# Performance work log

Measured on AMD Instinct MI355X. Metric: run time of the kernel, lower is better.

## Reference

```python
import jax, jax.numpy as jnp
import numpy as np

B, S, E, H = 1, 2048, 2048, 32
D = E // H  # head_dim = 64
QMAX = 127.0


def _ste(x, xq):
    # straight-through fake quant (forward = xq, grad = identity)
    return x + jax.lax.stop_gradient(xq - x)


def fake_quant_act(x):
    # per-tensor symmetric int8 fake quantization (QuantMatMul.quant_x*/act quantizer)
    scale = jnp.maximum(jnp.max(jnp.abs(x)) / QMAX, 1e-8)
    xq = jnp.clip(jnp.round(x / scale), -128.0, QMAX) * scale
    return _ste(x, xq)


def fake_quant_weight(w):
    # per-output-channel symmetric int8 fake quantization (weight quantizer)
    scale = jnp.maximum(jnp.max(jnp.abs(w), axis=1, keepdims=True) / QMAX, 1e-8)
    wq = jnp.clip(jnp.round(w / scale), -128.0, QMAX) * scale
    return _ste(w, wq)


def rope_cos_sin(seq_len, dim):
    inv_freq = 1.0 / (10000.0 ** (jnp.arange(0, dim, 2, dtype=jnp.float32) / dim))
    t = jnp.arange(seq_len, dtype=jnp.float32)
    freqs = jnp.outer(t, inv_freq)            # [S, D/2]
    emb = jnp.concatenate([freqs, freqs], -1)  # [S, D]
    return jnp.cos(emb), jnp.sin(emb)


def rotate_half(x):
    x1, x2 = jnp.split(x, 2, axis=-1)
    return jnp.concatenate([-x2, x1], axis=-1)


def setup_inputs() -> dict:
    key = jax.random.key(0)
    ks = jax.random.split(key, 5)
    return {
        "hidden_states": jax.random.normal(ks[0], (B, S, E), dtype=jnp.float32),
        "w_q": jax.random.normal(ks[1], (E, E), dtype=jnp.float32) * 0.02,
        "w_k": jax.random.normal(ks[2], (E, E), dtype=jnp.float32) * 0.02,
        "w_v": jax.random.normal(ks[3], (E, E), dtype=jnp.float32) * 0.02,
        "w_o": jax.random.normal(ks[4], (E, E), dtype=jnp.float32) * 0.02,
    }


def reference(hidden_states, w_q, w_k, w_v, w_o):
    scaling = D ** -0.5
    # quantized projections (QuantLinear: fake-quant weight, no input quant for q/k/v)
    q = hidden_states @ fake_quant_weight(w_q).T * scaling
    k = hidden_states @ fake_quant_weight(w_k).T
    v = hidden_states @ fake_quant_weight(w_v).T
    # qkt_matmul.quant_x1/quant_x2, pv_matmul.quant_x2
    q = fake_quant_act(q)
    k = fake_quant_act(k)
    v = fake_quant_act(v)
    # [B,S,E] -> [B,H,S,D]
    q = q.reshape(B, S, H, D).transpose(0, 2, 1, 3)
    k = k.reshape(B, S, H, D).transpose(0, 2, 1, 3)
    v = v.reshape(B, S, H, D).transpose(0, 2, 1, 3)
    # rotary embedding
    cos, sin = rope_cos_sin(S, D)
    cos = cos[None, None]
    sin = sin[None, None]
    q = q * cos + rotate_half(q) * sin
    k = k * cos + rotate_half(k) * sin
    # QK^T (already scaled via q) + causal mask
    scores = jnp.einsum("bhsd,bhtd->bhst", q, k)  # [B,H,S,S]
    causal = jnp.tril(jnp.ones((S, S), dtype=bool))
    scores = jnp.where(causal[None, None], scores, jnp.finfo(scores.dtype).min)
    probs = jax.nn.softmax(scores.astype(jnp.float32), axis=-1).astype(q.dtype)
    # PV matmul (v already fake-quantized)
    out = jnp.einsum("bhst,bhtd->bhsd", probs, v)
    out = out.transpose(0, 2, 1, 3).reshape(B, S, E)
    # o_proj: QuantLinear with input quant enabled
    out = fake_quant_act(out) @ fake_quant_weight(w_o).T
    return out
```

## Files before the change

### kernel.cpp

```cpp
#include <hip/hip_runtime.h>
#include <hip/hip_bf16.h>
#include <hip/hip_fp16.h>

#define S_LEN 2048
#define E_DIM 2048
#define H_NUM 32
#define D_DIM 64

typedef __attribute__((ext_vector_type(8))) short short8;
typedef __attribute__((ext_vector_type(4))) short short4v;
typedef __attribute__((ext_vector_type(4))) float f32x4;
typedef __attribute__((ext_vector_type(4))) int i32x4;

__device__ __forceinline__ unsigned short f2h(float f) {
  return __builtin_bit_cast(unsigned short, (_Float16)f);
}

__device__ __forceinline__ float h2f(unsigned short u) {
  return (float)__builtin_bit_cast(_Float16, u);
}

__device__ __forceinline__ float fq1(float x, float invs, float scale) {
  return fminf(fmaxf(rintf(x * invs), -128.f), 127.f) * scale;
}

__device__ __forceinline__ int q8(float x, float invs) {
  return min(max((int)rintf(x * invs), -128), 127);
}

__device__ __forceinline__ void gload_lds16(const void* g, void* l) {
  __builtin_amdgcn_global_load_lds((const __attribute__((address_space(1))) void*)g,
                                   (__attribute__((address_space(3))) void*)l, 16, 0, 0);
}

__device__ __forceinline__ f32x4 mfma16h(short8 a, short8 b, f32x4 c) {
  return __builtin_amdgcn_mfma_f32_16x16x32_f16(a, b, c, 0, 0, 0);
}

__device__ __forceinline__ i32x4 mfma16i8(i32x4 a, i32x4 b, i32x4 c) {
  return __builtin_amdgcn_mfma_i32_16x16x64_i8(a, b, c, 0, 0, 0);
}

#define VMW4() asm volatile("s_waitcnt vmcnt(4)" ::: "memory")
#define VMW3() asm volatile("s_waitcnt vmcnt(3)" ::: "memory")
#define VMW2() asm volatile("s_waitcnt vmcnt(2)" ::: "memory")
#define VMW0() asm volatile("s_waitcnt vmcnt(0)" ::: "memory")
#define BARR() asm volatile("s_barrier" ::: "memory")

__global__ void k_prep(const float* __restrict__ hs,
                       const float* __restrict__ w_q, const float* __restrict__ w_k,
                       const float* __restrict__ w_v, const float* __restrict__ w_o,
                       unsigned short* __restrict__ hsb, unsigned short* __restrict__ wq_all,
                       signed char* __restrict__ wo_i8, float* __restrict__ wsc,
                       unsigned* __restrict__ sc, float2* __restrict__ trig) {
  const int b = blockIdx.x;
  if (b < 4096) {
    int i = b * 256 + threadIdx.x;
    float4 v = ((const float4*)hs)[i];
    ushort4 r;
    r.x = f2h(v.x); r.y = f2h(v.y); r.z = f2h(v.z); r.w = f2h(v.w);
    ((ushort4*)hsb)[i] = r;
    return;
  }
  if (b >= 12288) {
    if (b == 12288) {
      if (threadIdx.x < 8) sc[threadIdx.x] = 0u;
      return;
    }
    int idx = (b - 12289) * 256 + threadIdx.x;
    int s = idx >> 5, i = idx & 31;
    float freq = exp2f(-(float)i * (13.287712379549449f / 32.f));
    float ang = (float)s * freq;
    float sn, cs;
    sincosf(ang, &sn, &cs);
    float2 t; t.x = cs; t.y = sn;
    trig[idx] = t;
    return;
  }
  __shared__ float wm[4];
  const int isWo = (b >= 10240);
  const int bb = isWo ? (b - 10240) : (b - 4096);
  const int wy = isWo ? 0 : (bb >> 11);
  const int wx = isWo ? bb : (bb & 2047);
  const float* w = isWo ? w_o : (wy == 0 ? w_q : wy == 1 ? w_k : w_v);
  const float* row = w + (size_t)wx * E_DIM;
  float4 a = ((const float4*)row)[threadIdx.x * 2];
  float4 bq = ((const float4*)row)[threadIdx.x * 2 + 1];
  float m = fmaxf(fmaxf(fmaxf(fabsf(a.x), fabsf(a.y)), fmaxf(fabsf(a.z), fabsf(a.w))),
                  fmaxf(fmaxf(fabsf(bq.x), fabsf(bq.y)), fmaxf(fabsf(bq.z), fabsf(bq.w))));
#pragma unroll
  for (int off = 32; off; off >>= 1) m = fmaxf(m, __shfl_xor(m, off));
  if ((threadIdx.x & 63) == 0) wm[threadIdx.x >> 6] = m;
  __syncthreads();
  m = fmaxf(fmaxf(wm[0], wm[1]), fmaxf(wm[2], wm[3]));
  float scale = fmaxf(m * (1.f / 127.f), 1e-8f);
  float invs = 1.f / scale;
  if (isWo) {
    unsigned lo = (unsigned)(q8(a.x, invs) & 255) | ((unsigned)(q8(a.y, invs) & 255) << 8) |
                  ((unsigned)(q8(a.z, invs) & 255) << 16) | ((unsigned)(q8(a.w, invs) & 255) << 24);
    unsigned hi = (unsigned)(q8(bq.x, invs) & 255) | ((unsigned)(q8(bq.y, invs) & 255) << 8) |
                  ((unsigned)(q8(bq.z, invs) & 255) << 16) | ((unsigned)(q8(bq.w, invs) & 255) << 24);
    uint2 pk; pk.x = lo; pk.y = hi;
    ((uint2*)(wo_i8 + (size_t)wx * E_DIM))[threadIdx.x] = pk;
    if (threadIdx.x == 0) wsc[wx] = scale;
  } else {
    unsigned short* orow = wq_all + (size_t)wy * E_DIM * E_DIM + (size_t)wx * E_DIM;
    ushort4 r0, r1;
    r0.x = f2h(fq1(a.x, invs, scale)); r0.y = f2h(fq1(a.y, invs, scale));
    r0.z = f2h(fq1(a.z, invs, scale)); r0.w = f2h(fq1(a.w, invs, scale));
    r1.x = f2h(fq1(bq.x, invs, scale)); r1.y = f2h(fq1(bq.y, invs, scale));
    r1.z = f2h(fq1(bq.z, invs, scale)); r1.w = f2h(fq1(bq.w, invs, scale));
    ((ushort4*)orow)[threadIdx.x * 2] = r0;
    ((ushort4*)orow)[threadIdx.x * 2 + 1] = r1;
  }
}

__global__ __launch_bounds__(256, 3)
void k_gemm_qkv(const unsigned short* __restrict__ A, const unsigned short* __restrict__ Bt,
                unsigned short* __restrict__ C, unsigned* __restrict__ amax, float alpha_q) {
  __shared__ char lds[49152];
  const int K = 2048, NT = 64;
  const int lin = blockIdx.z * 256 + blockIdx.y * 16 + blockIdx.x;
  const int swz = (lin & 7) * 96 + (lin >> 3);
  const int z = swz >> 8;
  const int iby = (swz >> 4) & 15;
  const int ibx = swz & 15;
  const unsigned short* Bz = Bt + (size_t)z * E_DIM * E_DIM;
  unsigned short* Cz = C + (size_t)z * S_LEN * E_DIM;
  const float alpha = (z == 0) ? alpha_q : 1.0f;

  const int tid = threadIdx.x;
  const int wv = tid >> 6, ln = tid & 63;
  const int wm = wv >> 1, wn = wv & 1;
  const size_t bm = (size_t)ibx * 128, bn = (size_t)iby * 128;
  const int arow = ln & 15, gsl = ln >> 4;

  int abyte[4], bbyte[4];
#pragma unroll
  for (int i = 0; i < 4; ++i) {
    int ra = wm * 64 + i * 16 + arow;
    abyte[i] = ra * 64 + ((gsl ^ ((ra >> 1) & 3)) * 16);
    int rb = wn * 64 + i * 16 + arow;
    bbyte[i] = rb * 64 + ((gsl ^ ((rb >> 1) & 3)) * 16);
  }

  const int srow = tid >> 2;
  const int sl = (tid & 3) ^ ((srow >> 1) & 3);
  const unsigned short* Ast = A + (bm + srow) * (size_t)K + sl * 8;
  const unsigned short* Bst = Bz + (bn + srow) * (size_t)K + sl * 8;

#define STG(T, dst) do { if ((T) < NT) { \
    size_t go = (size_t)(T) * 32; \
    gload_lds16(Ast + go, (dst) + wv * 1024); \
    gload_lds16(Ast + go + (size_t)64 * K, (dst) + 4096 + wv * 1024); \
    gload_lds16(Bst + go, (dst) + 8192 + wv * 1024); \
    gload_lds16(Bst + go + (size_t)64 * K, (dst) + 12288 + wv * 1024); } } while (0)

  f32x4 acc[4][4];
#pragma unroll
  for (int i = 0; i < 4; ++i)
#pragma unroll
    for (int j = 0; j < 4; ++j) { acc[i][j][0] = 0.f; acc[i][j][1] = 0.f; acc[i][j][2] = 0.f; acc[i][j][3] = 0.f; }

  char* b0 = lds;
  char* b1 = lds + 16384;
  char* b2 = lds + 32768;

  STG(0, b0); STG(1, b1);
  VMW4();
  BARR();

#define ITER(T, bufR, bufS) do { \
    short8 af[4], bf[4]; \
    _Pragma("unroll") \
    for (int i = 0; i < 4; ++i) af[i] = *(const short8*)((bufR) + abyte[i]); \
    _Pragma("unroll") \
    for (int j = 0; j < 4; ++j) bf[j] = *(const short8*)((bufR) + 8192 + bbyte[j]); \
    STG((T) + 2, bufS); \
    __builtin_amdgcn_s_setprio(1); \
    _Pragma("unroll") \
    for (int i = 0; i < 4; ++i) \
      _Pragma("unroll") \
      for (int j = 0; j < 4; ++j) acc[i][j] = mfma16h(af[i], bf[j], acc[i][j]); \
    __builtin_amdgcn_s_setprio(0); \
    if ((T) == NT - 2) { VMW0(); } else if ((T) < NT - 2) { VMW4(); } \
    BARR(); } while (0)

#pragma unroll 1
  for (int t = 0; t < NT - 1; t += 3) {
    ITER(t, b0, b2);
    ITER(t + 1, b1, b0);
    ITER(t + 2, b2, b1);
  }
  ITER(NT - 1, b0, b2);
#undef ITER
#undef STG

  float amx = 0.f;
#pragma unroll
  for (int i = 0; i < 4; ++i) {
    size_t rowb = bm + wm * 64 + i * 16 + gsl * 4;
#pragma unroll
    for (int j = 0; j < 4; ++j) {
      size_t col = bn + wn * 64 + j * 16 + arow;
#pragma unroll
      for (int r = 0; r < 4; ++r) {
        float v = acc[i][j][r] * alpha;
        Cz[(rowb + r) * E_DIM + col] = f2h(v);
        amx = fmaxf(amx, fabsf(v));
      }
    }
  }
#pragma unroll
  for (int off = 32; off; off >>= 1) amx = fmaxf(amx, __shfl_xor(amx, off));
  if (ln == 0) atomicMax(amax + z, __float_as_uint(amx));
}

__global__ __launch_bounds__(256, 4)
void k_gemm_o(const signed char* __restrict__ A, const signed char* __restrict__ Bt,
              float* __restrict__ C, const unsigned* __restrict__ sc,
              const float* __restrict__ wsc) {
  __shared__ char lds[36864];
  const int K = 2048, NT = 32;
  const float sa = fmaxf(__uint_as_float(sc[3]) * (1.f / 127.f), 1e-8f);
  const int lin = blockIdx.y * 16 + blockIdx.x;
  const int swz = (lin & 7) * 64 + (lin >> 3);
  const int iby = swz >> 4;
  const int ibx = swz & 15;

  const int tid = threadIdx.x;
  const int wv = tid >> 6, ln = tid & 63;
  const int wm = wv >> 1, wn = wv & 1;
  const size_t bm = (size_t)ibx * 128, bn = (size_t)iby * 64;
  const int arow = ln & 15, gsl = ln >> 4;

  int abyte[4], bbyte[2];
#pragma unroll
  for (int i = 0; i < 4; ++i) {
    int ra = wm * 64 + i * 16 + arow;
    abyte[i] = ra * 64 + ((gsl ^ ((ra >> 1) & 3)) * 16);
  }
#pragma unroll
  for (int j = 0; j < 2; ++j) {
    int rb = wn * 32 + j * 16 + arow;
    bbyte[j] = rb * 64 + ((gsl ^ ((rb >> 1) & 3)) * 16);
  }

  const int srow = tid >> 2;
  const int sl = (tid & 3) ^ ((srow >> 1) & 3);
  const signed char* Ast = A + (bm + srow) * (size_t)K + sl * 16;
  const signed char* Bst = Bt + (bn + srow) * (size_t)K + sl * 16;

#define STG(T, dst) do { if ((T) < NT) { \
    size_t go = (size_t)(T) * 64; \
    gload_lds16(Ast + go, (dst) + wv * 1024); \
    gload_lds16(Ast + go + (size_t)64 * K, (dst) + 4096 + wv * 1024); \
    gload_lds16(Bst + go, (dst) + 8192 + wv * 1024); } } while (0)

  i32x4 acc[4][2];
#pragma unroll
  for (int i = 0; i < 4; ++i)
#pragma unroll
    for (int j = 0; j < 2; ++j) { acc[i][j][0] = 0; acc[i][j][1] = 0; acc[i][j][2] = 0; acc[i][j][3] = 0; }

  char* b0 = lds;
  char* b1 = lds + 12288;
  char* b2 = lds + 24576;

  STG(0, b0); STG(1, b1);
  VMW3();
  BARR();

#define ITER(T, bufR, bufS) do { \
    i32x4 af[4], bf[2]; \
    _Pragma("unroll") \
    for (int i = 0; i < 4; ++i) af[i] = *(const i32x4*)((bufR) + abyte[i]); \
    _Pragma("unroll") \
    for (int j = 0; j < 2; ++j) bf[j] = *(const i32x4*)((bufR) + 8192 + bbyte[j]); \
    STG((T) + 2, bufS); \
    __builtin_amdgcn_s_setprio(1); \
    _Pragma("unroll") \
    for (int i = 0; i < 4; ++i) \
      _Pragma("unroll") \
      for (int j = 0; j < 2; ++j) acc[i][j] = mfma16i8(af[i], bf[j], acc[i][j]); \
    __builtin_amdgcn_s_setprio(0); \
    if ((T) == NT - 2) { VMW0(); } else if ((T) < NT - 2) { VMW3(); } \
    BARR(); } while (0)

#pragma unroll 1
  for (int t = 0; t + 2 < NT; t += 3) {
    ITER(t, b0, b2);
    ITER(t + 1, b1, b0);
    ITER(t + 2, b2, b1);
  }
  ITER(NT - 2, b0, b2);
  ITER(NT - 1, b1, b0);
#undef ITER
#undef STG

#pragma unroll
  for (int i = 0; i < 4; ++i) {
    size_t rowb = bm + wm * 64 + i * 16 + gsl * 4;
#pragma unroll
    for (int j = 0; j < 2; ++j) {
      size_t col = bn + wn * 32 + j * 16 + arow;
      float s = sa * wsc[col];
#pragma unroll
      for (int r = 0; r < 4; ++r)
        C[(rowb + r) * E_DIM + col] = (float)acc[i][j][r] * s;
    }
  }
}

__global__ void k_rvt(const unsigned short* __restrict__ qkv,
                      unsigned short* __restrict__ Qh, unsigned short* __restrict__ Kh,
                      unsigned short* __restrict__ Vt, const unsigned* __restrict__ sc,
                      const float2* __restrict__ trig) {
  __shared__ float tb[64][65];
  const int z = blockIdx.z;
  if (z < 2) {
    const unsigned short* x = qkv + (z ? 4194304 : 0);
    unsigned short* out = z ? Kh : Qh;
    float scale = fmaxf(__uint_as_float(sc[z]) * (1.f / 127.f), 1e-8f);
    float invs = 1.f / scale;
    int h = blockIdx.y;
    int s = blockIdx.x * 8 + (threadIdx.x >> 5);
    int i = threadIdx.x & 31;
    size_t base = (size_t)s * E_DIM + h * 64 + i;
    float x0 = h2f(x[base]);
    float x1 = h2f(x[base + 32]);
    float q0 = fq1(x0, invs, scale);
    float q1 = fq1(x1, invs, scale);
    float2 t = trig[s * 32 + i];
    size_t ob = (size_t)h * S_LEN * D_DIM + (size_t)s * D_DIM + i;
    out[ob] = f2h(q0 * t.x - q1 * t.y);
    out[ob + 32] = f2h(q1 * t.x + q0 * t.y);
    return;
  }
  if (blockIdx.x >= 32) return;
  const unsigned short* v = qkv + 2 * 4194304;
  float scale = fmaxf(__uint_as_float(sc[2]) * (1.f / 127.f), 1e-8f);
  float invs = 1.f / scale;
  int s0 = blockIdx.x * 64, h = blockIdx.y;
#pragma unroll
  for (int l = 0; l < 16; ++l) {
    int idx = threadIdx.x + l * 256;
    int r = idx >> 6, c = idx & 63;
    float x = h2f(v[(size_t)(s0 + r) * E_DIM + h * 64 + c]);
    tb[r][c] = fq1(x, invs, scale);
  }
  __syncthreads();
#pragma unroll
  for (int l = 0; l < 16; ++l) {
    int idx = threadIdx.x + l * 256;
    int d = idx >> 6, s = idx & 63;
    Vt[(size_t)h * D_DIM * S_LEN + (size_t)d * S_LEN + s0 + s] = f2h(tb[s][d]);
  }
}

__global__ __launch_bounds__(256, 4)
void k_attn(const unsigned short* __restrict__ Qh, const unsigned short* __restrict__ Kh,
            const unsigned short* __restrict__ Vt, unsigned short* __restrict__ att,
            unsigned* __restrict__ amax) {
  __shared__ char Kbuf[2 * 8192];
  __shared__ char Vbuf[2 * 8192];
  __shared__ __align__(16) char Pb[8192];
  const int L = blockIdx.x;
  const int h = L & 31;
  const int qc = 31 - (L >> 5);
  const int nt = qc + 1;
  const int tid = threadIdx.x;
  const int wv = tid >> 6, ln = tid & 63;
  const int arow = ln & 15, gsl = ln >> 4;
  const unsigned short* Qb = Qh + (size_t)h * S_LEN * D_DIM;
  const unsigned short* Kb = Kh + (size_t)h * S_LEN * D_DIM;
  const unsigned short* Vb = Vt + (size_t)h * D_DIM * S_LEN;
  const int qr = qc * 64 + wv * 16;

  const int srow0 = tid >> 3, sch0 = (tid & 7) ^ (srow0 & 7);
  const int srow1 = 32 + (tid >> 3), sch1 = (tid & 7) ^ (srow1 & 7);

#define STAGEK(T, B) do { char* kd = Kbuf + (B) * 8192; const int tb_ = (T) * 64; \
    gload_lds16(Kb + (size_t)(tb_ + srow0) * D_DIM + sch0 * 8, kd + wv * 1024); \
    gload_lds16(Kb + (size_t)(tb_ + srow1) * D_DIM + sch1 * 8, kd + 4096 + wv * 1024); } while (0)
#define STAGEV(T, B) do { char* vd = Vbuf + (B) * 8192; const int tb_ = (T) * 64; \
    gload_lds16(Vb + (size_t)srow0 * S_LEN + tb_ + sch0 * 8, vd + wv * 1024); \
    gload_lds16(Vb + (size_t)srow1 * S_LEN + tb_ + sch1 * 8, vd + 4096 + wv * 1024); } while (0)

  short8 qa0 = *(const short8*)(Qb + (size_t)(qr + arow) * D_DIM + gsl * 8);
  short8 qa1 = *(const short8*)(Qb + (size_t)(qr + arow) * D_DIM + 32 + gsl * 8);

  f32x4 o[4];
  float mrow = -INFINITY, lrow = 0.f;
#pragma unroll
  for (int d = 0; d < 4; ++d) { o[d][0] = 0.f; o[d][1] = 0.f; o[d][2] = 0.f; o[d][3] = 0.f; }

  STAGEK(0, 0);
  STAGEV(0, 0);
  if (nt > 1) { STAGEK(1, 1); STAGEV(1, 1); VMW4(); } else { VMW0(); }
  BARR();

  char* Pw = Pb + wv * 2048 + arow * 128;
  const int arw7 = arow & 7;

#pragma unroll 1
  for (int t = 0; t < nt; ++t) {
    if (t >= 1 && t + 1 < nt) { STAGEK(t + 1, (t + 1) & 1); STAGEV(t + 1, (t + 1) & 1); }
    char* kb = Kbuf + (t & 1) * 8192;
    char* vb = Vbuf + (t & 1) * 8192;

    short8 kf[4][2];
#pragma unroll
    for (int kvb = 0; kvb < 4; ++kvb) {
      int row = kvb * 16 + arow;
      int sw = (row & 7) << 4;
      kf[kvb][0] = *(const short8*)(kb + row * 128 + ((gsl * 16) ^ sw));
      kf[kvb][1] = *(const short8*)(kb + row * 128 + ((64 + gsl * 16) ^ sw));
    }
    f32x4 s4[4];
#pragma unroll
    for (int kvb = 0; kvb < 4; ++kvb) {
      s4[kvb][0] = 0.f; s4[kvb][1] = 0.f; s4[kvb][2] = 0.f; s4[kvb][3] = 0.f;
    }
#pragma unroll
    for (int kvb = 0; kvb < 4; ++kvb) {
      s4[kvb] = mfma16h(kf[kvb][0], qa0, s4[kvb]);
      s4[kvb] = mfma16h(kf[kvb][1], qa1, s4[kvb]);
    }

    const int t0 = t * 64;
    const int qrow = qr + arow;
    if (t0 + 63 > qrow) {
#pragma unroll
      for (int kvb = 0; kvb < 4; ++kvb) {
        int colb = t0 + kvb * 16 + gsl * 4;
#pragma unroll
        for (int r = 0; r < 4; ++r)
          if (colb + r > qrow) s4[kvb][r] = -INFINITY;
      }
    }

    float smax = s4[0][0];
#pragma unroll
    for (int kvb = 0; kvb < 4; ++kvb)
#pragma unroll
      for (int r = 0; r < 4; ++r) smax = fmaxf(smax, s4[kvb][r]);
    smax = fmaxf(smax, __shfl_xor(smax, 16));
    smax = fmaxf(smax, __shfl_xor(smax, 32));

    float mn = fmaxf(mrow, smax);
    float corr = __expf(mrow - mn);
    mrow = mn;

    float rs = 0.f;
    float p[4][4];
#pragma unroll
    for (int kvb = 0; kvb < 4; ++kvb)
#pragma unroll
      for (int r = 0; r < 4; ++r) {
        p[kvb][r] = __expf(s4[kvb][r] - mn);
        rs += p[kvb][r];
      }
    rs += __shfl_xor(rs, 16);
    rs += __shfl_xor(rs, 32);
    lrow = lrow * corr + rs;

    float corr_r[4];
#pragma unroll
    for (int r = 0; r < 4; ++r) corr_r[r] = __shfl(corr, gsl * 4 + r);
#pragma unroll
    for (int d = 0; d < 4; ++d)
#pragma unroll
      for (int r = 0; r < 4; ++r) o[d][r] *= corr_r[r];

    __builtin_amdgcn_wave_barrier();
#pragma unroll
    for (int kvb = 0; kvb < 4; ++kvb) {
      short4v pw;
      pw[0] = (short)f2h(p[kvb][0]);
      pw[1] = (short)f2h(p[kvb][1]);
      pw[2] = (short)f2h(p[kvb][2]);
      pw[3] = (short)f2h(p[kvb][3]);
      const int u = kvb * 2 + (gsl >> 1);
      *(short4v*)(Pw + ((u ^ arw7) << 4) + ((gsl & 1) << 3)) = pw;
    }
    __builtin_amdgcn_wave_barrier();
    short8 pa0 = *(const short8*)(Pw + ((gsl ^ arw7) << 4));
    short8 pa1 = *(const short8*)(Pw + (((4 + gsl) ^ arw7) << 4));
    __builtin_amdgcn_wave_barrier();

    short8 vf[4][2];
#pragma unroll
    for (int d = 0; d < 4; ++d) {
      int row = d * 16 + arow;
      int sw = (row & 7) << 4;
      vf[d][0] = *(const short8*)(vb + row * 128 + ((gsl * 16) ^ sw));
      vf[d][1] = *(const short8*)(vb + row * 128 + ((64 + gsl * 16) ^ sw));
    }
#pragma unroll
    for (int d = 0; d < 4; ++d) {
      o[d] = mfma16h(pa0, vf[d][0], o[d]);
      o[d] = mfma16h(pa1, vf[d][1], o[d]);
    }

    VMW0();
    BARR();
  }
#undef STAGEK
#undef STAGEV

  float amx = 0.f;
  float invl = 1.f / lrow;
  float invl_r[4];
#pragma unroll
  for (int r = 0; r < 4; ++r) invl_r[r] = __shfl(invl, gsl * 4 + r);
#pragma unroll
  for (int r = 0; r < 4; ++r) {
    size_t row = (size_t)(qr + gsl * 4 + r);
#pragma unroll
    for (int d = 0; d < 4; ++d) {
      float v = o[d][r] * invl_r[r];
      att[row * E_DIM + h * 64 + d * 16 + arow] = f2h(v);
      amx = fmaxf(amx, fabsf(v));
    }
  }

#pragma unroll
  for (int off = 32; off; off >>= 1) amx = fmaxf(amx, __shfl_xor(amx, off));
  if (ln == 0) atomicMax(amax + 3, __float_as_uint(amx));
}

__global__ void k_quant_act_i8(const unsigned short* __restrict__ in, uint2* __restrict__ out,
                               const unsigned* __restrict__ sc, int idx) {
  float scale = fmaxf(__uint_as_float(sc[idx]) * (1.f / 127.f), 1e-8f);
  float invs = 1.f / scale;
  int i = blockIdx.x * blockDim.x + threadIdx.x;
  short8 v = ((const short8*)in)[i];
  unsigned lo = 0, hi = 0;
#pragma unroll
  for (int e = 0; e < 4; ++e)
    lo |= (unsigned)(q8(h2f((unsigned short)v[e]), invs) & 255) << (8 * e);
#pragma unroll
  for (int e = 0; e < 4; ++e)
    hi |= (unsigned)(q8(h2f((unsigned short)v[4 + e]), invs) & 255) << (8 * e);
  uint2 pk; pk.x = lo; pk.y = hi;
  out[i] = pk;
}

extern "C" void kernel_launch(void* const* d_in, const int* in_sizes, int n_in,
                              void* d_out, int out_size, void* d_ws, size_t ws_size,
                              hipStream_t stream) {
  const float* hs = (const float*)d_in[0];
  const float* w_q = (const float*)d_in[1];
  const float* w_k = (const float*)d_in[2];
  const float* w_v = (const float*)d_in[3];
  const float* w_o = (const float*)d_in[4];

  char* ws = (char*)d_ws;
  unsigned short* wq_all = (unsigned short*)(ws);
  signed char* wo_i8 = (signed char*)(ws + 25165824);
  float* wsc = (float*)(ws + 29360128);
  float2* trig = (float2*)(ws + 30408704);
  unsigned short* hsb = (unsigned short*)(ws + 33554432);
  unsigned short* qkv16 = (unsigned short*)(ws + 41943040);
  unsigned short* att = qkv16;
  signed char* aq_i8 = (signed char*)(ws + 67108864);
  unsigned short* Qh = (unsigned short*)(ws + 92274688);
  unsigned short* Kh = (unsigned short*)(ws + 100663296);
  unsigned short* Vt = (unsigned short*)(ws + 109051904);
  unsigned* sc = (unsigned*)(ws + 117440512);

  k_prep<<<12545, 256, 0, stream>>>(hs, w_q, w_k, w_v, w_o, hsb, wq_all, wo_i8, wsc, sc, trig);
  k_gemm_qkv<<<dim3(16, 16, 3), 256, 0, stream>>>(hsb, wq_all, qkv16, sc, 0.125f);
  k_rvt<<<dim3(256, 32, 3), 256, 0, stream>>>(qkv16, Qh, Kh, Vt, sc, trig);
  k_attn<<<1024, 256, 0, stream>>>(Qh, Kh, Vt, att, sc);
  k_quant_act_i8<<<2048, 256, 0, stream>>>(att, (uint2*)aq_i8, sc, 3);
  k_gemm_o<<<dim3(16, 32), 256, 0, stream>>>(aq_i8, wo_i8, (float*)d_out, sc, wsc);
}
```

Measured before the change: 197.1 us.

## Enlarge QKV GEMM tile to 256x256 with 8 waves and double-buffered K64 stages

Reworks the fused QKV projection GEMM from 128x128 tiles with 4 waves and a triple-buffered K32 pipeline into 256x256 tiles with 8 waves, 128KB LDS, and double-buffered K64 stages split into four sub-phases. Each sub-phase interleaves LDS fragment reads, asynchronous global-to-LDS loads and MFMA bursts, separated by barriers and scheduling fences. The goal is higher arithmetic intensity per loaded byte and less global/L2 traffic. In exchange there are far fewer blocks (192 for 256 CUs), so occupancy and CU coverage drop and barrier overhead rises.

```diff
diff --git a/kernel.cpp b/kernel.cpp
--- a/kernel.cpp
+++ b/kernel.cpp
@@ -43,9 +43,10 @@
 
 #define VMW4() asm volatile("s_waitcnt vmcnt(4)" ::: "memory")
 #define VMW3() asm volatile("s_waitcnt vmcnt(3)" ::: "memory")
-#define VMW2() asm volatile("s_waitcnt vmcnt(2)" ::: "memory")
 #define VMW0() asm volatile("s_waitcnt vmcnt(0)" ::: "memory")
 #define BARR() asm volatile("s_barrier" ::: "memory")
+#define LGKM0() asm volatile("s_waitcnt lgkmcnt(0)" ::: "memory")
+#define SCHB() __builtin_amdgcn_sched_barrier(0)
 
 __global__ void k_prep(const float* __restrict__ hs,
                        const float* __restrict__ w_q, const float* __restrict__ w_k,
@@ -115,91 +116,126 @@
   }
 }
 
-__global__ __launch_bounds__(256, 3)
+__global__ __launch_bounds__(512, 2)
 void k_gemm_qkv(const unsigned short* __restrict__ A, const unsigned short* __restrict__ Bt,
                 unsigned short* __restrict__ C, unsigned* __restrict__ amax, float alpha_q) {
-  __shared__ char lds[49152];
-  const int K = 2048, NT = 64;
-  const int lin = blockIdx.z * 256 + blockIdx.y * 16 + blockIdx.x;
-  const int swz = (lin & 7) * 96 + (lin >> 3);
-  const int z = swz >> 8;
-  const int iby = (swz >> 4) & 15;
-  const int ibx = swz & 15;
+  __shared__ char lds[131072];
+  const int K = 2048, NT = 32;
+  const int lin = blockIdx.x;
+  const int swz = (lin & 7) * 24 + (lin >> 3);
+  const int z = swz >> 6;
+  const int t64 = swz & 63;
+  const int iby = t64 >> 3;
+  const int ibx = t64 & 7;
   const unsigned short* Bz = Bt + (size_t)z * E_DIM * E_DIM;
   unsigned short* Cz = C + (size_t)z * S_LEN * E_DIM;
   const float alpha = (z == 0) ? alpha_q : 1.0f;
 
   const int tid = threadIdx.x;
   const int wv = tid >> 6, ln = tid & 63;
-  const int wm = wv >> 1, wn = wv & 1;
-  const size_t bm = (size_t)ibx * 128, bn = (size_t)iby * 128;
+  const int wm = wv >> 2, wn = wv & 3;
+  const size_t bm = (size_t)ibx * 256, bn = (size_t)iby * 256;
   const int arow = ln & 15, gsl = ln >> 4;
 
-  int abyte[4], bbyte[4];
-#pragma unroll
-  for (int i = 0; i < 4; ++i) {
-    int ra = wm * 64 + i * 16 + arow;
-    abyte[i] = ra * 64 + ((gsl ^ ((ra >> 1) & 3)) * 16);
-    int rb = wn * 64 + i * 16 + arow;
-    bbyte[i] = rb * 64 + ((gsl ^ ((rb >> 1) & 3)) * 16);
+  int abyte[8], bbyte[4];
+#pragma unroll
+  for (int i = 0; i < 8; ++i) {
+    int r = wm * 128 + i * 16 + arow;
+    abyte[i] = r * 64 + ((gsl ^ ((r >> 1) & 3)) * 16);
+  }
+#pragma unroll
+  for (int j = 0; j < 4; ++j) {
+    int r = wn * 64 + j * 16 + arow;
+    bbyte[j] = 32768 + r * 64 + ((gsl ^ ((r >> 1) & 3)) * 16);
   }
 
   const int srow = tid >> 2;
-  const int sl = (tid & 3) ^ ((srow >> 1) & 3);
-  const unsigned short* Ast = A + (bm + srow) * (size_t)K + sl * 8;
-  const unsigned short* Bst = Bz + (bn + srow) * (size_t)K + sl * 8;
-
-#define STG(T, dst) do { if ((T) < NT) { \
-    size_t go = (size_t)(T) * 32; \
-    gload_lds16(Ast + go, (dst) + wv * 1024); \
-    gload_lds16(Ast + go + (size_t)64 * K, (dst) + 4096 + wv * 1024); \
-    gload_lds16(Bst + go, (dst) + 8192 + wv * 1024); \
-    gload_lds16(Bst + go + (size_t)64 * K, (dst) + 12288 + wv * 1024); } } while (0)
-
-  f32x4 acc[4][4];
-#pragma unroll
-  for (int i = 0; i < 4; ++i)
+  const int scc = (tid & 3) ^ ((tid >> 3) & 3);
+  const unsigned short* Asrc = A + (bm + srow) * (size_t)K + scc * 8;
+  const unsigned short* Bsrc = Bz + (bn + srow) * (size_t)K + scc * 8;
+  const int ldst = tid * 16;
+
+#define STGA(T, S) do { \
+    char* d_ = lds + ((T) & 1) * 65536 + (S) * 16384 + ldst; \
+    const unsigned short* s_ = Asrc + (T) * 64 + (S) * 32; \
+    gload_lds16(s_, d_); \
+    gload_lds16(s_ + (size_t)128 * K, d_ + 8192); } while (0)
+#define STGB(T, S) do { \
+    char* d_ = lds + ((T) & 1) * 65536 + 32768 + (S) * 16384 + ldst; \
+    const unsigned short* s_ = Bsrc + (T) * 64 + (S) * 32; \
+    gload_lds16(s_, d_); \
+    gload_lds16(s_ + (size_t)128 * K, d_ + 8192); } while (0)
+
+  f32x4 acc[8][4];
+#pragma unroll
+  for (int i = 0; i < 8; ++i)
 #pragma unroll
     for (int j = 0; j < 4; ++j) { acc[i][j][0] = 0.f; acc[i][j][1] = 0.f; acc[i][j][2] = 0.f; acc[i][j][3] = 0.f; }
 
-  char* b0 = lds;
-  char* b1 = lds + 16384;
-  char* b2 = lds + 32768;
-
-  STG(0, b0); STG(1, b1);
+  STGA(0, 0); STGB(0, 0); STGA(0, 1); STGB(0, 1);
   VMW4();
   BARR();
 
-#define ITER(T, bufR, bufS) do { \
-    short8 af[4], bf[4]; \
-    _Pragma("unroll") \
-    for (int i = 0; i < 4; ++i) af[i] = *(const short8*)((bufR) + abyte[i]); \
-    _Pragma("unroll") \
-    for (int j = 0; j < 4; ++j) bf[j] = *(const short8*)((bufR) + 8192 + bbyte[j]); \
-    STG((T) + 2, bufS); \
+#define TILE(BUF, DS, T1, W2X, W4X) do { \
+    char* bp_ = lds + (BUF); \
+    short8 af_[4], bf_[4], ag_[4]; \
+     \
+    _Pragma("unroll") for (int i = 0; i < 4; ++i) af_[i] = *(const short8*)(bp_ + abyte[i]); \
+    _Pragma("unroll") for (int j = 0; j < 4; ++j) bf_[j] = *(const short8*)(bp_ + bbyte[j]); \
+    if (DS) STGA(T1, 0); \
+    BARR(); LGKM0(); SCHB(); \
     __builtin_amdgcn_s_setprio(1); \
-    _Pragma("unroll") \
-    for (int i = 0; i < 4; ++i) \
-      _Pragma("unroll") \
-      for (int j = 0; j < 4; ++j) acc[i][j] = mfma16h(af[i], bf[j], acc[i][j]); \
+    _Pragma("unroll") for (int i = 0; i < 4; ++i) \
+      _Pragma("unroll") for (int j = 0; j < 4; ++j) acc[i][j] = mfma16h(af_[i], bf_[j], acc[i][j]); \
     __builtin_amdgcn_s_setprio(0); \
-    if ((T) == NT - 2) { VMW0(); } else if ((T) < NT - 2) { VMW4(); } \
-    BARR(); } while (0)
+    BARR(); \
+     \
+    _Pragma("unroll") for (int i = 0; i < 4; ++i) ag_[i] = *(const short8*)(bp_ + abyte[4 + i]); \
+    if (DS) STGB(T1, 0); \
+    BARR(); LGKM0(); SCHB(); \
+    __builtin_amdgcn_s_setprio(1); \
+    _Pragma("unroll") for (int i = 0; i < 4; ++i) \
+      _Pragma("unroll") for (int j = 0; j < 4; ++j) acc[4 + i][j] = mfma16h(ag_[i], bf_[j], acc[4 + i][j]); \
+    __builtin_amdgcn_s_setprio(0); \
+    W2X; \
+    BARR(); \
+     \
+    _Pragma("unroll") for (int i = 0; i < 4; ++i) af_[i] = *(const short8*)(bp_ + 16384 + abyte[i]); \
+    _Pragma("unroll") for (int j = 0; j < 4; ++j) bf_[j] = *(const short8*)(bp_ + 16384 + bbyte[j]); \
+    if (DS) STGA(T1, 1); \
+    BARR(); LGKM0(); SCHB(); \
+    __builtin_amdgcn_s_setprio(1); \
+    _Pragma("unroll") for (int i = 0; i < 4; ++i) \
+      _Pragma("unroll") for (int j = 0; j < 4; ++j) acc[i][j] = mfma16h(af_[i], bf_[j], acc[i][j]); \
+    __builtin_amdgcn_s_setprio(0); \
+    BARR(); \
+     \
+    _Pragma("unroll") for (int i = 0; i < 4; ++i) ag_[i] = *(const short8*)(bp_ + 16384 + abyte[4 + i]); \
+    if (DS) STGB(T1, 1); \
+    BARR(); LGKM0(); SCHB(); \
+    __builtin_amdgcn_s_setprio(1); \
+    _Pragma("unroll") for (int i = 0; i < 4; ++i) \
+      _Pragma("unroll") for (int j = 0; j < 4; ++j) acc[4 + i][j] = mfma16h(ag_[i], bf_[j], acc[4 + i][j]); \
+    __builtin_amdgcn_s_setprio(0); \
+    W4X; \
+    BARR(); \
+  } while (0)
 
 #pragma unroll 1
-  for (int t = 0; t < NT - 1; t += 3) {
-    ITER(t, b0, b2);
-    ITER(t + 1, b1, b0);
-    ITER(t + 2, b2, b1);
-  }
-  ITER(NT - 1, b0, b2);
-#undef ITER
-#undef STG
+  for (int t = 0; t < NT - 2; t += 2) {
+    TILE(0, 1, t + 1, VMW4(), VMW4());
+    TILE(65536, 1, t + 2, VMW4(), VMW4());
+  }
+  TILE(0, 1, NT - 1, VMW4(), VMW4());
+  TILE(65536, 0, 0, VMW0(), (void)0);
+#undef TILE
+#undef STGA
+#undef STGB
 
   float amx = 0.f;
 #pragma unroll
-  for (int i = 0; i < 4; ++i) {
-    size_t rowb = bm + wm * 64 + i * 16 + gsl * 4;
+  for (int i = 0; i < 8; ++i) {
+    size_t rowb = bm + wm * 128 + i * 16 + gsl * 4;
 #pragma unroll
     for (int j = 0; j < 4; ++j) {
       size_t col = bn + wn * 64 + j * 16 + arow;
@@ -571,7 +607,7 @@
   unsigned* sc = (unsigned*)(ws + 117440512);
 
   k_prep<<<12545, 256, 0, stream>>>(hs, w_q, w_k, w_v, w_o, hsb, wq_all, wo_i8, wsc, sc, trig);
-  k_gemm_qkv<<<dim3(16, 16, 3), 256, 0, stream>>>(hsb, wq_all, qkv16, sc, 0.125f);
+  k_gemm_qkv<<<dim3(192), 512, 0, stream>>>(hsb, wq_all, qkv16, sc, 0.125f);
   k_rvt<<<dim3(256, 32, 3), 256, 0, stream>>>(qkv16, Qh, Kh, Vt, sc, trig);
   k_attn<<<1024, 256, 0, stream>>>(Qh, Kh, Vt, att, sc);
   k_quant_act_i8<<<2048, 256, 0, stream>>>(att, (uint2*)aq_i8, sc, 3);
```

After: 187.2 us. 1.05x faster.
